# Optimization experiments

Hardware: AMD Instinct MI355X
Metric: run time of the kernel (lower is better)

## Reference

```python
import jax, jax.numpy as jnp
from jax import lax
import numpy as np

WS = 4          # window_size
DIM = 8         # per-head dim
HEADS = 32      # in_channels // dim
TOT = 256       # heads * dim
CIN = 256
COUT = 256
NS = 1          # len(scales), scales=(5,)
BN_EPS = 1e-5


def _avg_pool5(x):
    # AvgPool2d(kernel=5, stride=1, pad=2, count_include_pad=True) on NCHW
    s = lax.reduce_window(x, 0.0, lax.add, (1, 1, 5, 5), (1, 1, 1, 1),
                          [(0, 0), (0, 0), (2, 2), (2, 2)])
    return s / 25.0


def setup_inputs() -> dict:
    key = jax.random.key(0)
    k0, k1, k2 = jax.random.split(key, 3)
    B, H, W = 4, 192, 192
    x = jax.random.normal(k0, (B, CIN, H, W), jnp.float32)
    qkv_w = jax.random.normal(k1, (3 * TOT, CIN), jnp.float32) * 0.02
    proj_w = jax.random.normal(k2, (COUT, TOT * (1 + NS)), jnp.float32) * 0.02
    bn_gamma = jnp.ones((COUT,), jnp.float32)
    bn_beta = jnp.zeros((COUT,), jnp.float32)
    bn_mean = jnp.zeros((COUT,), jnp.float32)
    bn_var = jnp.ones((COUT,), jnp.float32)
    return {"x": x, "qkv_w": qkv_w, "proj_w": proj_w,
            "bn_gamma": bn_gamma, "bn_beta": bn_beta,
            "bn_mean": bn_mean, "bn_var": bn_var}


def reference(x, qkv_w, proj_w, bn_gamma, bn_beta, bn_mean, bn_var):
    B, C, H, W = x.shape
    ws = WS
    Hn, Wn = H // ws, W // ws
    # window partition: (B, C, H, W) -> (B*Hn*Wn, C, ws, ws)
    xw = x.reshape(B, C, Hn, ws, Wn, ws).transpose(0, 2, 4, 1, 3, 5)
    xw = xw.reshape(-1, C, ws, ws)
    N = xw.shape[0]
    # qkv 1x1 conv (no bias/norm/act)
    qkv = jnp.einsum('nchw,oc->nohw', xw, qkv_w)        # (N, 768, ws, ws)
    pooled = _avg_pool5(qkv)
    msq = jnp.concatenate([qkv, pooled], axis=1)        # (N, 1536, ws, ws)
    # (N, G=heads*(1+NS), 3*dim, ws*ws) -> (N, G, ws*ws, 3*dim)
    msq = msq.reshape(N, -1, 3 * DIM, ws * ws).transpose(0, 1, 3, 2)
    q = jax.nn.relu(msq[..., :DIM])                     # (N, G, L, d)
    k = jax.nn.relu(msq[..., DIM:2 * DIM])
    v = msq[..., 2 * DIM:]
    v = jnp.pad(v, ((0, 0), (0, 0), (0, 0), (0, 1)), constant_values=1.0)  # (N,G,L,d+1)
    kv = jnp.einsum('ngld,nglm->ngdm', k, v)            # (N, G, d, d+1)
    out = jnp.einsum('ngld,ngdm->nglm', q, kv)          # (N, G, L, d+1)
    out = out[..., :-1] / (out[..., -1:] + 1e-15)
    out = out.transpose(0, 1, 3, 2).reshape(N, -1, ws, ws)  # (N, G*d, ws, ws)
    Cw = out.shape[1]
    # window reverse: (B*Hn*Wn, Cw, ws, ws) -> (B, Cw, H, W)
    out = out.reshape(B, Hn, Wn, Cw, ws, ws).transpose(0, 3, 1, 4, 2, 5)
    out = out.reshape(B, Cw, H, W)
    # proj: 1x1 conv + BatchNorm2d (inference)
    y = jnp.einsum('nchw,oc->nohw', out, proj_w)
    inv = bn_gamma / jnp.sqrt(bn_var + BN_EPS)
    y = y * inv[None, :, None, None] + (bn_beta - bn_mean * inv)[None, :, None, None]
    return y
```

## Files before the change

kernel.cpp:

```cpp
#include <hip/hip_runtime.h>

#define HN 48
#define WN 48
#define CIN_ 256
#define H_ 192
#define W_ 192
#define COUT_ 256

#define PROJ_N (256 * 512)

#define DOT4(a, xv, wv) a += xv.x*wv.x + xv.y*wv.y + xv.z*wv.z + xv.w*wv.w

typedef __attribute__((ext_vector_type(8))) short bf16x8;
typedef __attribute__((ext_vector_type(4))) float f32x4;

__device__ __forceinline__ unsigned short f2b(float f) {
    unsigned int u = __float_as_uint(f);
    u = u + 0x7FFFu + ((u >> 16) & 1u);
    return (unsigned short)(u >> 16);
}
__device__ __forceinline__ float b2f(unsigned short h) {
    return __uint_as_float(((unsigned int)h) << 16);
}

__global__ __launch_bounds__(256) void prep_weights(const float* __restrict__ proj_w,
                                                    unsigned short* __restrict__ ws) {
    const int idx = blockIdx.x * 256 + threadIdx.x;
    if (idx < PROJ_N) {
        const float v = proj_w[idx];
        const unsigned short h = f2b(v);
        ws[idx] = h;
        ws[PROJ_N + idx] = f2b(v - b2f(h));
    }
}

__global__ __launch_bounds__(256, 1)
void wmsa_fused(const float* __restrict__ x, const float* __restrict__ qkv_w,
                const unsigned short* __restrict__ wp_h, const unsigned short* __restrict__ wp_l,
                const float* __restrict__ bn_g, const float* __restrict__ bn_b,
                const float* __restrict__ bn_m, const float* __restrict__ bn_v,
                float* __restrict__ y)
{
    __shared__ __align__(16) float xs[4][4164];
    __shared__ __align__(16) float wt[2][192 * 16];
    __shared__ __align__(16) float qs[384 * 16];
    __shared__ __align__(16) unsigned short af_hi[4][2048];
    __shared__ __align__(16) unsigned short af_lo[4][2048];

    const int t = threadIdx.x;
    const int bid = blockIdx.x;
    const int wb = (bid % 288) * 8 + (bid / 288);
    const int b = wb / 576;
    const int rem = wb % 576;
    const int hn = rem / 12, wn4 = rem % 12;
    const int h0 = hn * 4, w0 = wn4 * 16;

#pragma unroll
    for (int k = 0; k < 16; ++k) {
        const int idx = t + k * 256;
        const int wq = idx & 3;
        const int i = (idx >> 2) & 3;
        const int c = idx >> 4;
        const size_t ea = ((size_t)(b * CIN_ + c) * H_ + (h0 + i)) * (size_t)W_ + (w0 + wq * 4);
        const float4 r = *reinterpret_cast<const float4*>(x + ea);
        float* xw = xs[wq];
        xw[(i * 4 + 0) * 260 + c] = r.x;
        xw[(i * 4 + 1) * 260 + c] = r.y;
        xw[(i * 4 + 2) * 260 + c] = r.z;
        xw[(i * 4 + 3) * 260 + c] = r.w;
    }

    const int og = t >> 4;
    const int pix = t & 15;
    const int lane = t & 63;
    const int wv = t >> 6;
    const int lrow = lane & 15;
    const int lk = lane >> 4;

    f32x4 pacc[4][4];
#pragma unroll
    for (int i = 0; i < 4; ++i)
#pragma unroll
        for (int w = 0; w < 4; ++w) pacc[i][w] = (f32x4){0.f, 0.f, 0.f, 0.f};

    const int s0 = t, s1 = t + 256, s2 = t + 512;
    float4 stg0, stg1, stg2;

    __syncthreads();

    for (int pass = 0; pass < 4; ++pass) {
        float a[4][12];
#pragma unroll
        for (int w = 0; w < 4; ++w)
#pragma unroll
            for (int j = 0; j < 12; ++j) a[w][j] = 0.f;

        {
            const float* gw = qkv_w + (size_t)pass * 192 * 256;
            stg0 = *reinterpret_cast<const float4*>(gw + (s0 >> 2) * 256 + (s0 & 3) * 4);
            stg1 = *reinterpret_cast<const float4*>(gw + (s1 >> 2) * 256 + (s1 & 3) * 4);
            stg2 = *reinterpret_cast<const float4*>(gw + (s2 >> 2) * 256 + (s2 & 3) * 4);
            *reinterpret_cast<float4*>(&wt[0][s0 * 4]) = stg0;
            *reinterpret_cast<float4*>(&wt[0][s1 * 4]) = stg1;
            *reinterpret_cast<float4*>(&wt[0][s2 * 4]) = stg2;
        }
        __syncthreads();

        for (int cc = 0; cc < 16; ++cc) {
            const int buf = cc & 1;
            if (cc < 15) {
                const float* gw = qkv_w + (size_t)pass * 192 * 256 + (cc + 1) * 16;
                stg0 = *reinterpret_cast<const float4*>(gw + (s0 >> 2) * 256 + (s0 & 3) * 4);
                stg1 = *reinterpret_cast<const float4*>(gw + (s1 >> 2) * 256 + (s1 & 3) * 4);
                stg2 = *reinterpret_cast<const float4*>(gw + (s2 >> 2) * 256 + (s2 & 3) * 4);
            }
            const int xoff = pix * 260 + cc * 16;
#pragma unroll
            for (int c4 = 0; c4 < 4; ++c4) {
                const float4 xv0 = *reinterpret_cast<const float4*>(&xs[0][xoff + c4 * 4]);
                const float4 xv1 = *reinterpret_cast<const float4*>(&xs[1][xoff + c4 * 4]);
                const float4 xv2 = *reinterpret_cast<const float4*>(&xs[2][xoff + c4 * 4]);
                const float4 xv3 = *reinterpret_cast<const float4*>(&xs[3][xoff + c4 * 4]);
                const float* wbase = &wt[buf][og * 16 + c4 * 4];
#pragma unroll
                for (int j = 0; j < 12; ++j) {
                    const float4 wvj = *reinterpret_cast<const float4*>(&wbase[j * 256]);
                    DOT4(a[0][j], xv0, wvj);
                    DOT4(a[1][j], xv1, wvj);
                    DOT4(a[2][j], xv2, wvj);
                    DOT4(a[3][j], xv3, wvj);
                }
            }
            if (cc < 15) {
                *reinterpret_cast<float4*>(&wt[buf ^ 1][s0 * 4]) = stg0;
                *reinterpret_cast<float4*>(&wt[buf ^ 1][s1 * 4]) = stg1;
                *reinterpret_cast<float4*>(&wt[buf ^ 1][s2 * 4]) = stg2;
            }
            __syncthreads();
        }

#pragma unroll
        for (int w = 0; w < 4; ++w) {
#pragma unroll
            for (int j = 0; j < 12; ++j)
                qs[(og + 16 * j) * 16 + pix] = a[w][j];
            __syncthreads();

            if (t < 192) {
                const float4* sr = reinterpret_cast<const float4*>(&qs[t * 16]);
                const float4 r0 = sr[0], r1 = sr[1], r2 = sr[2], r3 = sr[3];
                float col[4], tmp0[4], tmp3[4];
                {
                    const float c0 = r0.x + r1.x + r2.x + r3.x;
                    const float c1 = r0.y + r1.y + r2.y + r3.y;
                    const float c2 = r0.z + r1.z + r2.z + r3.z;
                    const float c3 = r0.w + r1.w + r2.w + r3.w;
                    col[0] = c0; col[1] = c1; col[2] = c2; col[3] = c3;
                    tmp0[0] = c0 - r3.x; tmp0[1] = c1 - r3.y; tmp0[2] = c2 - r3.z; tmp0[3] = c3 - r3.w;
                    tmp3[0] = c0 - r0.x; tmp3[1] = c1 - r0.y; tmp3[2] = c2 - r0.z; tmp3[3] = c3 - r0.w;
                }
                float4* pr = reinterpret_cast<float4*>(&qs[(192 + t) * 16]);
                const float k25 = 1.f / 25.f;
#pragma unroll
                for (int i = 0; i < 4; ++i) {
                    const float* tr = (i == 0) ? tmp0 : ((i == 3) ? tmp3 : col);
                    const float hs = tr[0] + tr[1] + tr[2] + tr[3];
                    float4 o;
                    o.x = (hs - tr[3]) * k25;
                    o.y = hs * k25;
                    o.z = hs * k25;
                    o.w = (hs - tr[0]) * k25;
                    pr[i] = o;
                }
            }
            __syncthreads();

            {
                const int grp = t >> 4;
                const int l = t & 15;
                const int base = (grp < 8) ? (grp * 24 * 16) : ((192 + (grp - 8) * 24) * 16);

                float qd[8], kd[8], vm[8];
#pragma unroll
                for (int d = 0; d < 8; ++d) qd[d] = fmaxf(0.f, qs[base + d * 16 + l]);
#pragma unroll
                for (int d = 0; d < 8; ++d) kd[d] = fmaxf(0.f, qs[base + (8 + d) * 16 + l]);
#pragma unroll
                for (int m = 0; m < 8; ++m) vm[m] = qs[base + (16 + m) * 16 + l];

                float kv[8][9];
#pragma unroll
                for (int d = 0; d < 8; ++d) {
#pragma unroll
                    for (int m = 0; m < 8; ++m) kv[d][m] = kd[d] * vm[m];
                    kv[d][8] = kd[d];
                }
#pragma unroll
                for (int off = 1; off <= 8; off <<= 1)
#pragma unroll
                    for (int d = 0; d < 8; ++d)
#pragma unroll
                        for (int m = 0; m < 9; ++m)
                            kv[d][m] += __shfl_xor(kv[d][m], off, 64);

                float o8 = 0.f;
#pragma unroll
                for (int d = 0; d < 8; ++d) o8 += qd[d] * kv[d][8];
                const float den = 1.f / (o8 + 1e-15f);

                bf16x8 sh, sl;
#pragma unroll
                for (int m = 0; m < 8; ++m) {
                    float om = 0.f;
#pragma unroll
                    for (int d = 0; d < 8; ++d) om += qd[d] * kv[d][m];
                    const float vvv = om * den;
                    const unsigned short h = f2b(vvv);
                    sh[m] = (short)h;
                    sl[m] = (short)f2b(vvv - b2f(h));
                }
                *reinterpret_cast<bf16x8*>(&af_hi[w][t * 8]) = sh;
                *reinterpret_cast<bf16x8*>(&af_lo[w][t * 8]) = sl;
            }
            __syncthreads();
        }

#pragma unroll
        for (int s = 0; s < 4; ++s) {
            const int u = ((s * 4 + lk) * 16 + lrow) * 8;
            const bf16x8 bh0 = *reinterpret_cast<const bf16x8*>(&af_hi[0][u]);
            const bf16x8 bh1 = *reinterpret_cast<const bf16x8*>(&af_hi[1][u]);
            const bf16x8 bh2 = *reinterpret_cast<const bf16x8*>(&af_hi[2][u]);
            const bf16x8 bh3 = *reinterpret_cast<const bf16x8*>(&af_hi[3][u]);
            const bf16x8 bl0 = *reinterpret_cast<const bf16x8*>(&af_lo[0][u]);
            const bf16x8 bl1 = *reinterpret_cast<const bf16x8*>(&af_lo[1][u]);
            const bf16x8 bl2 = *reinterpret_cast<const bf16x8*>(&af_lo[2][u]);
            const bf16x8 bl3 = *reinterpret_cast<const bf16x8*>(&af_lo[3][u]);
            const int colbase = ((s < 2) ? (pass * 64 + s * 32)
                                         : (256 + pass * 64 + (s - 2) * 32)) + lk * 8;
#pragma unroll
            for (int tt = 0; tt < 4; ++tt) {
                const int row = (wv * 4 + tt) * 16 + lrow;
                const bf16x8 ah = *reinterpret_cast<const bf16x8*>(wp_h + (size_t)row * 512 + colbase);
                const bf16x8 al = *reinterpret_cast<const bf16x8*>(wp_l + (size_t)row * 512 + colbase);
                pacc[tt][0] = __builtin_amdgcn_mfma_f32_16x16x32_bf16(ah, bh0, pacc[tt][0], 0, 0, 0);
                pacc[tt][0] = __builtin_amdgcn_mfma_f32_16x16x32_bf16(ah, bl0, pacc[tt][0], 0, 0, 0);
                pacc[tt][0] = __builtin_amdgcn_mfma_f32_16x16x32_bf16(al, bh0, pacc[tt][0], 0, 0, 0);
                pacc[tt][1] = __builtin_amdgcn_mfma_f32_16x16x32_bf16(ah, bh1, pacc[tt][1], 0, 0, 0);
                pacc[tt][1] = __builtin_amdgcn_mfma_f32_16x16x32_bf16(ah, bl1, pacc[tt][1], 0, 0, 0);
                pacc[tt][1] = __builtin_amdgcn_mfma_f32_16x16x32_bf16(al, bh1, pacc[tt][1], 0, 0, 0);
                pacc[tt][2] = __builtin_amdgcn_mfma_f32_16x16x32_bf16(ah, bh2, pacc[tt][2], 0, 0, 0);
                pacc[tt][2] = __builtin_amdgcn_mfma_f32_16x16x32_bf16(ah, bl2, pacc[tt][2], 0, 0, 0);
                pacc[tt][2] = __builtin_amdgcn_mfma_f32_16x16x32_bf16(al, bh2, pacc[tt][2], 0, 0, 0);
                pacc[tt][3] = __builtin_amdgcn_mfma_f32_16x16x32_bf16(ah, bh3, pacc[tt][3], 0, 0, 0);
                pacc[tt][3] = __builtin_amdgcn_mfma_f32_16x16x32_bf16(ah, bl3, pacc[tt][3], 0, 0, 0);
                pacc[tt][3] = __builtin_amdgcn_mfma_f32_16x16x32_bf16(al, bh3, pacc[tt][3], 0, 0, 0);
            }
        }
    }

    const int oc = t;
    const float inv = bn_g[oc] * __frsqrt_rn(bn_v[oc] + 1e-5f);
    const float bet2 = bn_b[oc] - bn_m[oc] * inv;
#pragma unroll
    for (int w = 0; w < 4; ++w) {
        __syncthreads();
#pragma unroll
        for (int tt = 0; tt < 4; ++tt) {
            const int c0 = (wv * 4 + tt) * 16 + lk * 4;
#pragma unroll
            for (int r = 0; r < 4; ++r)
                qs[(c0 + r) * 16 + lrow] = pacc[tt][w][r];
        }
        __syncthreads();
        const float* rowp = &qs[oc * 16];
#pragma unroll
        for (int i = 0; i < 4; ++i) {
            float4 s4;
            s4.x = rowp[i * 4 + 0] * inv + bet2;
            s4.y = rowp[i * 4 + 1] * inv + bet2;
            s4.z = rowp[i * 4 + 2] * inv + bet2;
            s4.w = rowp[i * 4 + 3] * inv + bet2;
            const size_t ea = ((size_t)(b * COUT_ + oc) * H_ + (h0 + i)) * (size_t)W_ + (w0 + w * 4);
            *reinterpret_cast<float4*>(y + ea) = s4;
        }
    }
}

extern "C" void kernel_launch(void* const* d_in, const int* in_sizes, int n_in,
                              void* d_out, int out_size, void* d_ws, size_t ws_size,
                              hipStream_t stream) {
    const float* x      = (const float*)d_in[0];
    const float* qkv_w  = (const float*)d_in[1];
    const float* proj_w = (const float*)d_in[2];
    const float* bn_g   = (const float*)d_in[3];
    const float* bn_b   = (const float*)d_in[4];
    const float* bn_m   = (const float*)d_in[5];
    const float* bn_v   = (const float*)d_in[6];
    float* y = (float*)d_out;

    unsigned short* ws = (unsigned short*)d_ws;
    prep_weights<<<dim3(512), dim3(256), 0, stream>>>(proj_w, ws);
    wmsa_fused<<<dim3(2304), dim3(256), 0, stream>>>(
        x, qkv_w, ws, ws + PROJ_N,
        bn_g, bn_b, bn_m, bn_v, y);
}
```

Before: 2.280 ms.

## Double threads per block and process two windows concurrently in attention phase

Raises the block size from 256 to 512 threads. Each thread now computes half as many qkv output channels, and two of the four windows go through pooling and linear attention at once, one per 256-thread half. The projection MFMA work is split across 8 waves instead of 4 and interleaved per window pair, and launch bounds ask for 2 blocks per CU. This cuts per-thread register pressure and adds parallelism, but LDS use per block changes and weight staging becomes uneven across threads.

```diff
diff --git a/kernel.cpp b/kernel.cpp
--- a/kernel.cpp
+++ b/kernel.cpp
@@ -34,7 +34,7 @@
     }
 }
 
-__global__ __launch_bounds__(256, 1)
+__global__ __launch_bounds__(512, 2)
 void wmsa_fused(const float* __restrict__ x, const float* __restrict__ qkv_w,
                 const unsigned short* __restrict__ wp_h, const unsigned short* __restrict__ wp_l,
                 const float* __restrict__ bn_g, const float* __restrict__ bn_b,
@@ -42,10 +42,10 @@
                 float* __restrict__ y)
 {
     __shared__ __align__(16) float xs[4][4164];
-    __shared__ __align__(16) float wt[2][192 * 16];
-    __shared__ __align__(16) float qs[384 * 16];
-    __shared__ __align__(16) unsigned short af_hi[4][2048];
-    __shared__ __align__(16) unsigned short af_lo[4][2048];
+    __shared__ __align__(16) float wt[2][3072];
+    __shared__ __align__(16) float qs[2][6144];
+    __shared__ __align__(16) unsigned short af_hi[2][2048];
+    __shared__ __align__(16) unsigned short af_lo[2][2048];
 
     const int t = threadIdx.x;
     const int bid = blockIdx.x;
@@ -56,8 +56,8 @@
     const int h0 = hn * 4, w0 = wn4 * 16;
 
 #pragma unroll
-    for (int k = 0; k < 16; ++k) {
-        const int idx = t + k * 256;
+    for (int k = 0; k < 8; ++k) {
+        const int idx = t + k * 512;
         const int wq = idx & 3;
         const int i = (idx >> 2) & 3;
         const int c = idx >> 4;
@@ -70,39 +70,39 @@
         xw[(i * 4 + 3) * 260 + c] = r.w;
     }
 
-    const int og = t >> 4;
+    const int og2 = t >> 4;
     const int pix = t & 15;
     const int lane = t & 63;
     const int wv = t >> 6;
     const int lrow = lane & 15;
     const int lk = lane >> 4;
-
-    f32x4 pacc[4][4];
-#pragma unroll
-    for (int i = 0; i < 4; ++i)
+    const int wsel = t >> 8;
+    const int th = t & 255;
+
+    f32x4 pacc[2][4];
+#pragma unroll
+    for (int i = 0; i < 2; ++i)
 #pragma unroll
         for (int w = 0; w < 4; ++w) pacc[i][w] = (f32x4){0.f, 0.f, 0.f, 0.f};
 
-    const int s0 = t, s1 = t + 256, s2 = t + 512;
-    float4 stg0, stg1, stg2;
+    const int s0 = t, s1 = 512 + t;
+    float4 stg0, stg1;
 
     __syncthreads();
 
     for (int pass = 0; pass < 4; ++pass) {
-        float a[4][12];
+        float a[4][6];
 #pragma unroll
         for (int w = 0; w < 4; ++w)
 #pragma unroll
-            for (int j = 0; j < 12; ++j) a[w][j] = 0.f;
+            for (int j = 0; j < 6; ++j) a[w][j] = 0.f;
 
         {
             const float* gw = qkv_w + (size_t)pass * 192 * 256;
             stg0 = *reinterpret_cast<const float4*>(gw + (s0 >> 2) * 256 + (s0 & 3) * 4);
-            stg1 = *reinterpret_cast<const float4*>(gw + (s1 >> 2) * 256 + (s1 & 3) * 4);
-            stg2 = *reinterpret_cast<const float4*>(gw + (s2 >> 2) * 256 + (s2 & 3) * 4);
+            if (t < 256) stg1 = *reinterpret_cast<const float4*>(gw + (s1 >> 2) * 256 + (s1 & 3) * 4);
             *reinterpret_cast<float4*>(&wt[0][s0 * 4]) = stg0;
-            *reinterpret_cast<float4*>(&wt[0][s1 * 4]) = stg1;
-            *reinterpret_cast<float4*>(&wt[0][s2 * 4]) = stg2;
+            if (t < 256) *reinterpret_cast<float4*>(&wt[0][s1 * 4]) = stg1;
         }
         __syncthreads();
 
@@ -111,8 +111,7 @@
             if (cc < 15) {
                 const float* gw = qkv_w + (size_t)pass * 192 * 256 + (cc + 1) * 16;
                 stg0 = *reinterpret_cast<const float4*>(gw + (s0 >> 2) * 256 + (s0 & 3) * 4);
-                stg1 = *reinterpret_cast<const float4*>(gw + (s1 >> 2) * 256 + (s1 & 3) * 4);
-                stg2 = *reinterpret_cast<const float4*>(gw + (s2 >> 2) * 256 + (s2 & 3) * 4);
+                if (t < 256) stg1 = *reinterpret_cast<const float4*>(gw + (s1 >> 2) * 256 + (s1 & 3) * 4);
             }
             const int xoff = pix * 260 + cc * 16;
 #pragma unroll
@@ -121,10 +120,10 @@
                 const float4 xv1 = *reinterpret_cast<const float4*>(&xs[1][xoff + c4 * 4]);
                 const float4 xv2 = *reinterpret_cast<const float4*>(&xs[2][xoff + c4 * 4]);
                 const float4 xv3 = *reinterpret_cast<const float4*>(&xs[3][xoff + c4 * 4]);
-                const float* wbase = &wt[buf][og * 16 + c4 * 4];
-#pragma unroll
-                for (int j = 0; j < 12; ++j) {
-                    const float4 wvj = *reinterpret_cast<const float4*>(&wbase[j * 256]);
+                const float* wbase = &wt[buf][og2 * 16 + c4 * 4];
+#pragma unroll
+                for (int j = 0; j < 6; ++j) {
+                    const float4 wvj = *reinterpret_cast<const float4*>(&wbase[j * 512]);
                     DOT4(a[0][j], xv0, wvj);
                     DOT4(a[1][j], xv1, wvj);
                     DOT4(a[2][j], xv2, wvj);
@@ -133,21 +132,23 @@
             }
             if (cc < 15) {
                 *reinterpret_cast<float4*>(&wt[buf ^ 1][s0 * 4]) = stg0;
-                *reinterpret_cast<float4*>(&wt[buf ^ 1][s1 * 4]) = stg1;
-                *reinterpret_cast<float4*>(&wt[buf ^ 1][s2 * 4]) = stg2;
+                if (t < 256) *reinterpret_cast<float4*>(&wt[buf ^ 1][s1 * 4]) = stg1;
             }
             __syncthreads();
         }
 
 #pragma unroll
-        for (int w = 0; w < 4; ++w) {
-#pragma unroll
-            for (int j = 0; j < 12; ++j)
-                qs[(og + 16 * j) * 16 + pix] = a[w][j];
+        for (int p = 0; p < 2; ++p) {
+#pragma unroll
+            for (int j = 0; j < 6; ++j) {
+                qs[0][(og2 + 32 * j) * 16 + pix] = a[2 * p + 0][j];
+                qs[1][(og2 + 32 * j) * 16 + pix] = a[2 * p + 1][j];
+            }
             __syncthreads();
 
-            if (t < 192) {
-                const float4* sr = reinterpret_cast<const float4*>(&qs[t * 16]);
+            if (th < 192) {
+                float* qsw = qs[wsel];
+                const float4* sr = reinterpret_cast<const float4*>(&qsw[th * 16]);
                 const float4 r0 = sr[0], r1 = sr[1], r2 = sr[2], r3 = sr[3];
                 float col[4], tmp0[4], tmp3[4];
                 {
@@ -159,7 +160,7 @@
                     tmp0[0] = c0 - r3.x; tmp0[1] = c1 - r3.y; tmp0[2] = c2 - r3.z; tmp0[3] = c3 - r3.w;
                     tmp3[0] = c0 - r0.x; tmp3[1] = c1 - r0.y; tmp3[2] = c2 - r0.z; tmp3[3] = c3 - r0.w;
                 }
-                float4* pr = reinterpret_cast<float4*>(&qs[(192 + t) * 16]);
+                float4* pr = reinterpret_cast<float4*>(&qsw[(192 + th) * 16]);
                 const float k25 = 1.f / 25.f;
 #pragma unroll
                 for (int i = 0; i < 4; ++i) {
@@ -176,17 +177,18 @@
             __syncthreads();
 
             {
-                const int grp = t >> 4;
-                const int l = t & 15;
+                const int grp = th >> 4;
+                const int l = th & 15;
+                const float* qsw = qs[wsel];
                 const int base = (grp < 8) ? (grp * 24 * 16) : ((192 + (grp - 8) * 24) * 16);
 
                 float qd[8], kd[8], vm[8];
 #pragma unroll
-                for (int d = 0; d < 8; ++d) qd[d] = fmaxf(0.f, qs[base + d * 16 + l]);
-#pragma unroll
-                for (int d = 0; d < 8; ++d) kd[d] = fmaxf(0.f, qs[base + (8 + d) * 16 + l]);
-#pragma unroll
-                for (int m = 0; m < 8; ++m) vm[m] = qs[base + (16 + m) * 16 + l];
+                for (int d = 0; d < 8; ++d) qd[d] = fmaxf(0.f, qsw[base + d * 16 + l]);
+#pragma unroll
+                for (int d = 0; d < 8; ++d) kd[d] = fmaxf(0.f, qsw[base + (8 + d) * 16 + l]);
+#pragma unroll
+                for (int m = 0; m < 8; ++m) vm[m] = qsw[base + (16 + m) * 16 + l];
 
                 float kv[8][9];
 #pragma unroll
@@ -219,61 +221,54 @@
                     sh[m] = (short)h;
                     sl[m] = (short)f2b(vvv - b2f(h));
                 }
-                *reinterpret_cast<bf16x8*>(&af_hi[w][t * 8]) = sh;
-                *reinterpret_cast<bf16x8*>(&af_lo[w][t * 8]) = sl;
+                *reinterpret_cast<bf16x8*>(&af_hi[wsel][th * 8]) = sh;
+                *reinterpret_cast<bf16x8*>(&af_lo[wsel][th * 8]) = sl;
             }
             __syncthreads();
-        }
-
-#pragma unroll
-        for (int s = 0; s < 4; ++s) {
-            const int u = ((s * 4 + lk) * 16 + lrow) * 8;
-            const bf16x8 bh0 = *reinterpret_cast<const bf16x8*>(&af_hi[0][u]);
-            const bf16x8 bh1 = *reinterpret_cast<const bf16x8*>(&af_hi[1][u]);
-            const bf16x8 bh2 = *reinterpret_cast<const bf16x8*>(&af_hi[2][u]);
-            const bf16x8 bh3 = *reinterpret_cast<const bf16x8*>(&af_hi[3][u]);
-            const bf16x8 bl0 = *reinterpret_cast<const bf16x8*>(&af_lo[0][u]);
-            const bf16x8 bl1 = *reinterpret_cast<const bf16x8*>(&af_lo[1][u]);
-            const bf16x8 bl2 = *reinterpret_cast<const bf16x8*>(&af_lo[2][u]);
-            const bf16x8 bl3 = *reinterpret_cast<const bf16x8*>(&af_lo[3][u]);
-            const int colbase = ((s < 2) ? (pass * 64 + s * 32)
-                                         : (256 + pass * 64 + (s - 2) * 32)) + lk * 8;
-#pragma unroll
-            for (int tt = 0; tt < 4; ++tt) {
-                const int row = (wv * 4 + tt) * 16 + lrow;
-                const bf16x8 ah = *reinterpret_cast<const bf16x8*>(wp_h + (size_t)row * 512 + colbase);
-                const bf16x8 al = *reinterpret_cast<const bf16x8*>(wp_l + (size_t)row * 512 + colbase);
-                pacc[tt][0] = __builtin_amdgcn_mfma_f32_16x16x32_bf16(ah, bh0, pacc[tt][0], 0, 0, 0);
-                pacc[tt][0] = __builtin_amdgcn_mfma_f32_16x16x32_bf16(ah, bl0, pacc[tt][0], 0, 0, 0);
-                pacc[tt][0] = __builtin_amdgcn_mfma_f32_16x16x32_bf16(al, bh0, pacc[tt][0], 0, 0, 0);
-                pacc[tt][1] = __builtin_amdgcn_mfma_f32_16x16x32_bf16(ah, bh1, pacc[tt][1], 0, 0, 0);
-                pacc[tt][1] = __builtin_amdgcn_mfma_f32_16x16x32_bf16(ah, bl1, pacc[tt][1], 0, 0, 0);
-                pacc[tt][1] = __builtin_amdgcn_mfma_f32_16x16x32_bf16(al, bh1, pacc[tt][1], 0, 0, 0);
-                pacc[tt][2] = __builtin_amdgcn_mfma_f32_16x16x32_bf16(ah, bh2, pacc[tt][2], 0, 0, 0);
-                pacc[tt][2] = __builtin_amdgcn_mfma_f32_16x16x32_bf16(ah, bl2, pacc[tt][2], 0, 0, 0);
-                pacc[tt][2] = __builtin_amdgcn_mfma_f32_16x16x32_bf16(al, bh2, pacc[tt][2], 0, 0, 0);
-                pacc[tt][3] = __builtin_amdgcn_mfma_f32_16x16x32_bf16(ah, bh3, pacc[tt][3], 0, 0, 0);
-                pacc[tt][3] = __builtin_amdgcn_mfma_f32_16x16x32_bf16(ah, bl3, pacc[tt][3], 0, 0, 0);
-                pacc[tt][3] = __builtin_amdgcn_mfma_f32_16x16x32_bf16(al, bh3, pacc[tt][3], 0, 0, 0);
+
+#pragma unroll
+            for (int s = 0; s < 4; ++s) {
+                const int u = ((s * 4 + lk) * 16 + lrow) * 8;
+                const bf16x8 bh0 = *reinterpret_cast<const bf16x8*>(&af_hi[0][u]);
+                const bf16x8 bl0 = *reinterpret_cast<const bf16x8*>(&af_lo[0][u]);
+                const bf16x8 bh1 = *reinterpret_cast<const bf16x8*>(&af_hi[1][u]);
+                const bf16x8 bl1 = *reinterpret_cast<const bf16x8*>(&af_lo[1][u]);
+                const int colbase = ((s < 2) ? (pass * 64 + s * 32)
+                                             : (256 + pass * 64 + (s - 2) * 32)) + lk * 8;
+#pragma unroll
+                for (int tt = 0; tt < 2; ++tt) {
+                    const int row = (wv * 2 + tt) * 16 + lrow;
+                    const bf16x8 ah = *reinterpret_cast<const bf16x8*>(wp_h + (size_t)row * 512 + colbase);
+                    const bf16x8 al = *reinterpret_cast<const bf16x8*>(wp_l + (size_t)row * 512 + colbase);
+                    pacc[tt][2*p+0] = __builtin_amdgcn_mfma_f32_16x16x32_bf16(ah, bh0, pacc[tt][2*p+0], 0, 0, 0);
+                    pacc[tt][2*p+0] = __builtin_amdgcn_mfma_f32_16x16x32_bf16(ah, bl0, pacc[tt][2*p+0], 0, 0, 0);
+                    pacc[tt][2*p+0] = __builtin_amdgcn_mfma_f32_16x16x32_bf16(al, bh0, pacc[tt][2*p+0], 0, 0, 0);
+                    pacc[tt][2*p+1] = __builtin_amdgcn_mfma_f32_16x16x32_bf16(ah, bh1, pacc[tt][2*p+1], 0, 0, 0);
+                    pacc[tt][2*p+1] = __builtin_amdgcn_mfma_f32_16x16x32_bf16(ah, bl1, pacc[tt][2*p+1], 0, 0, 0);
+                    pacc[tt][2*p+1] = __builtin_amdgcn_mfma_f32_16x16x32_bf16(al, bh1, pacc[tt][2*p+1], 0, 0, 0);
+                }
             }
         }
     }
 
-    const int oc = t;
+    const int oc = th;
     const float inv = bn_g[oc] * __frsqrt_rn(bn_v[oc] + 1e-5f);
     const float bet2 = bn_b[oc] - bn_m[oc] * inv;
 #pragma unroll
-    for (int w = 0; w < 4; ++w) {
+    for (int p = 0; p < 2; ++p) {
         __syncthreads();
 #pragma unroll
-        for (int tt = 0; tt < 4; ++tt) {
-            const int c0 = (wv * 4 + tt) * 16 + lk * 4;
-#pragma unroll
-            for (int r = 0; r < 4; ++r)
-                qs[(c0 + r) * 16 + lrow] = pacc[tt][w][r];
+        for (int tt = 0; tt < 2; ++tt) {
+            const int c0 = (wv * 2 + tt) * 16 + lk * 4;
+#pragma unroll
+            for (int r = 0; r < 4; ++r) {
+                qs[0][(c0 + r) * 16 + lrow] = pacc[tt][2 * p + 0][r];
+                qs[1][(c0 + r) * 16 + lrow] = pacc[tt][2 * p + 1][r];
+            }
         }
         __syncthreads();
-        const float* rowp = &qs[oc * 16];
+        const float* rowp = &qs[wsel][oc * 16];
+        const int wwin = 2 * p + wsel;
 #pragma unroll
         for (int i = 0; i < 4; ++i) {
             float4 s4;
@@ -281,7 +276,7 @@
             s4.y = rowp[i * 4 + 1] * inv + bet2;
             s4.z = rowp[i * 4 + 2] * inv + bet2;
             s4.w = rowp[i * 4 + 3] * inv + bet2;
-            const size_t ea = ((size_t)(b * COUT_ + oc) * H_ + (h0 + i)) * (size_t)W_ + (w0 + w * 4);
+            const size_t ea = ((size_t)(b * COUT_ + oc) * H_ + (h0 + i)) * (size_t)W_ + (w0 + wwin * 4);
             *reinterpret_cast<float4*>(y + ea) = s4;
         }
     }
@@ -301,7 +296,7 @@
 
     unsigned short* ws = (unsigned short*)d_ws;
     prep_weights<<<dim3(512), dim3(256), 0, stream>>>(proj_w, ws);
-    wmsa_fused<<<dim3(2304), dim3(256), 0, stream>>>(
+    wmsa_fused<<<dim3(2304), dim3(512), 0, stream>>>(
         x, qkv_w, ws, ws + PROJ_N,
         bn_g, bn_b, bn_m, bn_v, y);
 }
```

After: 2.116 ms. 1.08x faster.
